# Performance work log

Hardware: AMD Instinct MI355X
Metric: run time of the kernel (lower is better)

The kernel has to match this reference:

```python
import jax, jax.numpy as jnp
import numpy as np
import math

EPS = 1e-08
KERNEL = 3
PAD = KERNEL // 2


def setup_inputs() -> dict:
    key = jax.random.key(0)
    k1, k2, k3, k4 = jax.random.split(key, 4)
    B, C_in, C_out, H, W, S = 8, 512, 512, 64, 64, 512
    x = jax.random.normal(k1, (B, C_in, H, W), dtype=jnp.float32)
    style = jax.random.normal(k2, (B, S), dtype=jnp.float32)
    # modulation Linear: kaiming_normal fan_in linear => std = 1/sqrt(S); bias filled with 1
    w_mod = jax.random.normal(k3, (C_in, S), dtype=jnp.float32) / math.sqrt(S)
    b_mod = jnp.ones((C_in,), dtype=jnp.float32)
    # conv weight: randn / sqrt(in * k^2)
    weight = jax.random.normal(k4, (1, C_out, C_in, KERNEL, KERNEL), dtype=jnp.float32) / math.sqrt(C_in * KERNEL * KERNEL)
    return {"x": x, "style": style, "w_mod": w_mod, "b_mod": b_mod, "weight": weight}


def _modconv(x, style, w_mod, b_mod, weight):
    # style modulation: (B, S) @ (S, C_in) + bias -> (B, 1, C_in, 1, 1)
    s = style @ w_mod.T + b_mod
    w = weight * s[:, None, :, None, None]            # (B, C_out, C_in, k, k)
    # demodulate: rsqrt of sum of squares over (in, kh, kw)
    demod = jax.lax.rsqrt(jnp.sum(w * w, axis=(2, 3, 4)) + EPS)  # (B, C_out)
    w = w * demod[:, :, None, None, None]

    # groups=B conv == per-sample conv; vmap over batch
    def conv1(xb, wb):
        # xb: (C_in, H, W), wb: (C_out, C_in, k, k)
        return jax.lax.conv_general_dilated(
            xb[None], wb, window_strides=(1, 1),
            padding=[(PAD, PAD), (PAD, PAD)],
            dimension_numbers=("NCHW", "OIHW", "NCHW"))[0]

    return jax.vmap(conv1)(x, w)  # (B, C_out, H, W)


def reference(x, style, w_mod, b_mod, weight):
    return _modconv(x, style, w_mod, b_mod, weight)
```

## Files before the change

### kernel.cpp

```cpp
#include <hip/hip_runtime.h>
#include <hip/hip_bf16.h>

#define BATCH 8
#define CIN   512
#define COUT  512
#define HH    64
#define WW    64
#define SS    512
#define HP    66
#define WP    66
#define NPIX  (HH*WW)

typedef __bf16 bfrag  __attribute__((ext_vector_type(8)));
typedef float  f32x4  __attribute__((ext_vector_type(4)));
typedef unsigned short u16x8 __attribute__((ext_vector_type(8)));

__device__ __forceinline__ void async_copy16(const __hip_bfloat16* g, __hip_bfloat16* l) {
    __builtin_amdgcn_global_load_lds(
        (const __attribute__((address_space(1))) void*)g,
        (__attribute__((address_space(3))) void*)l,
        16, 0, 0);
}

__device__ __forceinline__ bool is_f32(const void* b_mod) {
    return ((const unsigned int*)b_mod)[0] == 0x3F800000u;
}

__global__ void k_prep(const void* __restrict__ style,
                       const void* __restrict__ w_mod,
                       const void* __restrict__ b_mod,
                       const void* __restrict__ weight,
                       float* __restrict__ s_out,
                       float* __restrict__ wsq,
                       __hip_bfloat16* __restrict__ Wt) {
    const bool f32 = is_f32(b_mod);
    if (blockIdx.x < 1024) {
        int tid = blockIdx.x * 256 + threadIdx.x;
        float sq = 0.f;
        if (f32) {
            const float* w = (const float*)weight + (size_t)tid * 9;
#pragma unroll
            for (int k = 0; k < 9; ++k) {
                float v = w[k];
                sq += v * v;
                Wt[k * (COUT * CIN) + tid] = __float2bfloat16(v);
            }
        } else {
            const __hip_bfloat16* w = (const __hip_bfloat16*)weight + (size_t)tid * 9;
#pragma unroll
            for (int k = 0; k < 9; ++k) {
                float v = __bfloat162float(w[k]);
                sq += v * v;
                Wt[k * (COUT * CIN) + tid] = w[k];
            }
        }
        wsq[tid] = sq;
    } else {
        int gw   = (blockIdx.x - 1024) * 4 + (threadIdx.x >> 6);
        int lane = threadIdx.x & 63;
        int b = gw >> 9, i = gw & 511;
        int base = lane * 8;
        float acc = 0.f;
        if (f32) {
            const float* st = (const float*)style + b * SS + base;
            const float* wm = (const float*)w_mod + i * SS + base;
#pragma unroll
            for (int j = 0; j < 8; ++j) acc += st[j] * wm[j];
        } else {
            const __hip_bfloat16* st = (const __hip_bfloat16*)style + b * SS + base;
            const __hip_bfloat16* wm = (const __hip_bfloat16*)w_mod + i * SS + base;
#pragma unroll
            for (int j = 0; j < 8; ++j)
                acc += __bfloat162float(st[j]) * __bfloat162float(wm[j]);
        }
#pragma unroll
        for (int off = 32; off; off >>= 1) acc += __shfl_down(acc, off);
        if (lane == 0) {
            float bias = f32 ? ((const float*)b_mod)[i]
                             : __bfloat162float(((const __hip_bfloat16*)b_mod)[i]);
            s_out[gw] = acc + bias;
        }
    }
}

__global__ void k_mid(const void* __restrict__ xv,
                      const float* __restrict__ s_buf,
                      const float* __restrict__ wsq,
                      const void* __restrict__ b_mod,
                      float* __restrict__ demod,
                      int b0, int nx, int do_demod,
                      __hip_bfloat16* __restrict__ xpad) {
    if ((int)blockIdx.x >= nx) {
        if (!do_demod) return;
        int gw   = ((int)blockIdx.x - nx) * 4 + (threadIdx.x >> 6);
        int lane = threadIdx.x & 63;
        int b = gw >> 9, o = gw & 511;
        int base = lane * 8;
        const float* sp = s_buf + b * CIN + base;
        const float* wp = wsq + o * CIN + base;
        float acc = 0.f;
#pragma unroll
        for (int j = 0; j < 8; ++j) {
            float sv = sp[j];
            acc += sv * sv * wp[j];
        }
#pragma unroll
        for (int off = 32; off; off >>= 1) acc += __shfl_down(acc, off);
        if (lane == 0) demod[gw] = rsqrtf(acc + 1e-8f);
        return;
    }
    const bool f32 = is_f32(b_mod);
    int ic = blockIdx.x & 15;
    int h  = (blockIdx.x >> 4) & 63;
    int bl = blockIdx.x >> 10;
    int b  = b0 + bl;
    int t  = threadIdx.x;
    int g  = t & 3;
    int w  = t >> 2;
    int ch0 = ic * 32 + g * 8;

    float sv[8];
#pragma unroll
    for (int j = 0; j < 8; ++j) sv[j] = s_buf[b * CIN + ch0 + j];

    u16x8 outv;
#pragma unroll
    for (int j = 0; j < 8; ++j) {
        size_t src = (size_t)(b * CIN + ch0 + j) * NPIX + h * WW + w;
        float xval = f32 ? ((const float*)xv)[src]
                         : __bfloat162float(((const __hip_bfloat16*)xv)[src]);
        __hip_bfloat16 bv = __float2bfloat16(xval * sv[j]);
        outv[j] = *(unsigned short*)&bv;
    }
    size_t rowb = (size_t)(bl * HP + h + 1) * WP;
    *(u16x8*)(xpad + (rowb + (w + 1)) * CIN + ch0) = outv;

    u16x8 z = {};
    if (w == 0)  *(u16x8*)(xpad + (rowb + 0)  * CIN + ch0) = z;
    if (w == 63) *(u16x8*)(xpad + (rowb + 65) * CIN + ch0) = z;
    if (h == 0) {
        size_t r0 = (size_t)(bl * HP + 0) * WP;
        *(u16x8*)(xpad + (r0 + (w + 1)) * CIN + ch0) = z;
        if (w == 0)  *(u16x8*)(xpad + (r0 + 0)  * CIN + ch0) = z;
        if (w == 63) *(u16x8*)(xpad + (r0 + 65) * CIN + ch0) = z;
    }
    if (h == 63) {
        size_t r65 = (size_t)(bl * HP + 65) * WP;
        *(u16x8*)(xpad + (r65 + (w + 1)) * CIN + ch0) = z;
        if (w == 0)  *(u16x8*)(xpad + (r65 + 0)  * CIN + ch0) = z;
        if (w == 63) *(u16x8*)(xpad + (r65 + 65) * CIN + ch0) = z;
    }
}

__global__ __launch_bounds__(256, 2)
void k_conv(const __hip_bfloat16* __restrict__ Wt,
            const __hip_bfloat16* __restrict__ xpad,
            const float* __restrict__ demod,
            const void* __restrict__ b_mod, int b0,
            void* __restrict__ outv) {
    __shared__ __hip_bfloat16 sA[2][3][128 * 32];
    __shared__ __hip_bfloat16 sB[2][6144];

    const int tid  = threadIdx.x;
    const int wid  = tid >> 6;
    const int lane = tid & 63;
    const int p_tile = blockIdx.x;
    const int o_tile = blockIdx.y;
    const int bl     = blockIdx.z;
    const int b      = b0 + bl;

    const int o_base = o_tile * 128;
    const int h0     = p_tile * 2;
    const int p_base = p_tile * 128;

    const int sw = ((lane & 3) ^ ((lane >> 3) & 3)) * 8;

    const int arow0 = wid * 32 + (lane >> 2);
    const int arow1 = arow0 + 16;
    const int aoff0 = wid * 1024 + lane * 8;
    const int aoff1 = aoff0 + 512;
    const int asrc0 = (o_base + arow0) * CIN + sw;
    const int asrc1 = (o_base + arow1) * CIN + sw;

    int bdst[3], bsrc[3];
#pragma unroll
    for (int jj = 0; jj < 3; ++jj) {
        int j   = wid * 3 + jj;
        int pix = j * 16 + (lane >> 2);
        int pm  = pix < 131 ? pix : 131;
        int r   = (pm >= 66) ? 1 : 0;
        int c   = pm - (r ? 66 : 0);
        bdst[jj] = j * 512 + lane * 8;
        bsrc[jj] = ((bl * HP + h0 + r) * WP + c) * CIN + sw;
    }

    const int quad   = lane >> 4;
    const int l15    = lane & 15;
    const int wave_m = (wid >> 1) * 64;
    const int wave_n = (wid & 1) * 64;
    int afrag[4];
#pragma unroll
    for (int mt = 0; mt < 4; ++mt) {
        int row = wave_m + mt * 16 + l15;
        afrag[mt] = row * 32 + ((quad ^ ((l15 >> 1) & 3)) * 8);
    }
    int bfroff[4][3];
#pragma unroll
    for (int nt = 0; nt < 4; ++nt) {
        int n   = wave_n + nt * 16 + l15;
        int pr0 = (n >> 6) * 66 + (n & 63);
#pragma unroll
        for (int kw = 0; kw < 3; ++kw) {
            int pr = pr0 + kw;
            bfroff[nt][kw] = pr * 32 + ((quad ^ ((pr >> 1) & 3)) * 8);
        }
    }

    f32x4 acc[4][4];
#pragma unroll
    for (int mt = 0; mt < 4; ++mt)
#pragma unroll
        for (int nt = 0; nt < 4; ++nt)
            acc[mt][nt] = (f32x4)0.f;

    auto stage = [&](int buf, int it) {
        const int kh = it >> 4;
        const int i0 = (it & 15) << 5;
        const __hip_bfloat16* Wkh = Wt + kh * 3 * (COUT * CIN) + i0;
        const __hip_bfloat16* xr  = xpad + kh * (WP * CIN) + i0;
#pragma unroll
        for (int kw = 0; kw < 3; ++kw) {
            const __hip_bfloat16* Ap = Wkh + kw * (COUT * CIN);
            async_copy16(Ap + asrc0, &sA[buf][kw][aoff0]);
            async_copy16(Ap + asrc1, &sA[buf][kw][aoff1]);
        }
#pragma unroll
        for (int jj = 0; jj < 3; ++jj)
            async_copy16(xr + bsrc[jj], &sB[buf][bdst[jj]]);
    };

    auto compute = [&](int buf) {
        __builtin_amdgcn_s_setprio(1);
#pragma unroll
        for (int kw = 0; kw < 3; ++kw) {
            bfrag a[4], bb[4];
#pragma unroll
            for (int mt = 0; mt < 4; ++mt)
                a[mt] = *(const bfrag*)(&sA[buf][kw][afrag[mt]]);
#pragma unroll
            for (int nt = 0; nt < 4; ++nt)
                bb[nt] = *(const bfrag*)(&sB[buf][bfroff[nt][kw]]);
#pragma unroll
            for (int mt = 0; mt < 4; ++mt)
#pragma unroll
                for (int nt = 0; nt < 4; ++nt)
                    acc[mt][nt] = __builtin_amdgcn_mfma_f32_16x16x32_bf16(
                        a[mt], bb[nt], acc[mt][nt], 0, 0, 0);
        }
        __builtin_amdgcn_s_setprio(0);
    };

    stage(0, 0);
#pragma unroll 2
    for (int it = 0; it < 47; ++it) {
        stage((it + 1) & 1, it + 1);
        asm volatile("s_waitcnt vmcnt(9)" ::: "memory");
        __builtin_amdgcn_s_barrier();
        asm volatile("" ::: "memory");
        compute(it & 1);
        asm volatile("" ::: "memory");
        __builtin_amdgcn_s_barrier();
    }
    asm volatile("s_waitcnt vmcnt(0)" ::: "memory");
    __builtin_amdgcn_s_barrier();
    asm volatile("" ::: "memory");
    compute(1);

    const bool f32 = is_f32(b_mod);
#pragma unroll
    for (int mt = 0; mt < 4; ++mt) {
        const int o0r = o_base + wave_m + mt * 16 + quad * 4;
        float dm[4];
#pragma unroll
        for (int r = 0; r < 4; ++r) dm[r] = demod[b * COUT + o0r + r];
#pragma unroll
        for (int nt = 0; nt < 4; ++nt) {
            const int p = p_base + wave_n + nt * 16 + l15;
#pragma unroll
            for (int r = 0; r < 4; ++r) {
                float val = acc[mt][nt][r] * dm[r];
                size_t idx = (size_t)(b * COUT + o0r + r) * NPIX + p;
                if (f32) ((float*)outv)[idx] = val;
                else     ((__hip_bfloat16*)outv)[idx] = __float2bfloat16(val);
            }
        }
    }
}

extern "C" void kernel_launch(void* const* d_in, const int* in_sizes, int n_in,
                              void* d_out, int out_size, void* d_ws, size_t ws_size,
                              hipStream_t stream) {
    const void* x      = d_in[0];
    const void* style  = d_in[1];
    const void* w_mod  = d_in[2];
    const void* b_mod  = d_in[3];
    const void* weight = d_in[4];

    char* ws = (char*)d_ws;
    float*          s_buf = (float*)(ws + 4096);
    float*          demod = (float*)(ws + 20480);
    float*          wsq   = (float*)(ws + 36864);
    __hip_bfloat16* Wt    = (__hip_bfloat16*)(ws + 1085440);
    __hip_bfloat16* xpad  = (__hip_bfloat16*)(ws + 5804032);

    const size_t need_full = 5804032 + (size_t)BATCH * HP * WP * CIN * 2;
    const int group = (ws_size >= need_full) ? 8 : 4;

    k_prep<<<2048, 256, 0, stream>>>(style, w_mod, b_mod, weight, s_buf, wsq, Wt);

    for (int b0 = 0; b0 < BATCH; b0 += group) {
        const int nx = 1024 * group;
        const int do_demod = (b0 == 0) ? 1 : 0;
        const int nd = do_demod ? 1024 : 0;
        k_mid<<<nx + nd, 256, 0, stream>>>(x, s_buf, wsq, b_mod, demod,
                                           b0, nx, do_demod, xpad);
        k_conv<<<dim3(32, 4, group), 256, 0, stream>>>(Wt, xpad, demod, b_mod, b0, d_out);
    }
}
```

Baseline: 269.0 us.

## Load conv weight fragments directly from global memory and remap blocks per XCD

Drops the LDS staging of the modulated-weight (A) operand. Each wave now reads its A fragments straight from global memory into registers at the start of each compute step, and only the input (B) tile is still staged asynchronously through LDS. This shrinks LDS use, so the launch bound is raised to three blocks per CU. The 3D grid is also flattened into a 1D grid with an XCD-aware mapping, so that blocks sharing an output-channel tile land on the same XCD for L2 reuse. In exchange, the global A loads have no prefetch, so their latency may be exposed right before the MFMAs, and waves sharing rows issue duplicate loads.

After: 436.1 us. +62.1%, slower.

```diff
diff --git a/kernel.cpp b/kernel.cpp
--- a/kernel.cpp
+++ b/kernel.cpp
@@ -152,21 +152,24 @@
     }
 }
 
-__global__ __launch_bounds__(256, 2)
+__global__ __launch_bounds__(256, 3)
 void k_conv(const __hip_bfloat16* __restrict__ Wt,
             const __hip_bfloat16* __restrict__ xpad,
             const float* __restrict__ demod,
             const void* __restrict__ b_mod, int b0,
             void* __restrict__ outv) {
-    __shared__ __hip_bfloat16 sA[2][3][128 * 32];
     __shared__ __hip_bfloat16 sB[2][6144];
 
     const int tid  = threadIdx.x;
     const int wid  = tid >> 6;
     const int lane = tid & 63;
-    const int p_tile = blockIdx.x;
-    const int o_tile = blockIdx.y;
-    const int bl     = blockIdx.z;
+
+    const int id     = blockIdx.x;
+    const int xcd    = id & 7;
+    const int g      = id >> 3;
+    const int o_tile = xcd >> 1;
+    const int p_tile = (xcd & 1) * 16 + (g & 15);
+    const int bl     = g >> 4;
     const int b      = b0 + bl;
 
     const int o_base = o_tile * 128;
@@ -174,13 +177,6 @@
     const int p_base = p_tile * 128;
 
     const int sw = ((lane & 3) ^ ((lane >> 3) & 3)) * 8;
-
-    const int arow0 = wid * 32 + (lane >> 2);
-    const int arow1 = arow0 + 16;
-    const int aoff0 = wid * 1024 + lane * 8;
-    const int aoff1 = aoff0 + 512;
-    const int asrc0 = (o_base + arow0) * CIN + sw;
-    const int asrc1 = (o_base + arow1) * CIN + sw;
 
     int bdst[3], bsrc[3];
 #pragma unroll
@@ -198,12 +194,9 @@
     const int l15    = lane & 15;
     const int wave_m = (wid >> 1) * 64;
     const int wave_n = (wid & 1) * 64;
-    int afrag[4];
-#pragma unroll
-    for (int mt = 0; mt < 4; ++mt) {
-        int row = wave_m + mt * 16 + l15;
-        afrag[mt] = row * 32 + ((quad ^ ((l15 >> 1) & 3)) * 8);
-    }
+
+    const __hip_bfloat16* Arow = Wt + (size_t)(o_base + wave_m + l15) * CIN + quad * 8;
+
     int bfroff[4][3];
 #pragma unroll
     for (int nt = 0; nt < 4; ++nt) {
@@ -223,30 +216,29 @@
         for (int nt = 0; nt < 4; ++nt)
             acc[mt][nt] = (f32x4)0.f;
 
-    auto stage = [&](int buf, int it) {
+    auto stageB = [&](int buf, int it) {
         const int kh = it >> 4;
         const int i0 = (it & 15) << 5;
-        const __hip_bfloat16* Wkh = Wt + kh * 3 * (COUT * CIN) + i0;
-        const __hip_bfloat16* xr  = xpad + kh * (WP * CIN) + i0;
-#pragma unroll
-        for (int kw = 0; kw < 3; ++kw) {
-            const __hip_bfloat16* Ap = Wkh + kw * (COUT * CIN);
-            async_copy16(Ap + asrc0, &sA[buf][kw][aoff0]);
-            async_copy16(Ap + asrc1, &sA[buf][kw][aoff1]);
-        }
+        const __hip_bfloat16* xr = xpad + kh * (WP * CIN) + i0;
 #pragma unroll
         for (int jj = 0; jj < 3; ++jj)
             async_copy16(xr + bsrc[jj], &sB[buf][bdst[jj]]);
     };
 
-    auto compute = [&](int buf) {
+    auto compute = [&](int buf, int it) {
+        const int kh = it >> 4;
+        const int i0 = (it & 15) << 5;
+        const __hip_bfloat16* Ap = Arow + kh * 3 * (COUT * CIN) + i0;
+        bfrag a[3][4];
+#pragma unroll
+        for (int kw = 0; kw < 3; ++kw)
+#pragma unroll
+            for (int mt = 0; mt < 4; ++mt)
+                a[kw][mt] = *(const bfrag*)(Ap + kw * (COUT * CIN) + mt * 16 * CIN);
         __builtin_amdgcn_s_setprio(1);
 #pragma unroll
         for (int kw = 0; kw < 3; ++kw) {
-            bfrag a[4], bb[4];
-#pragma unroll
-            for (int mt = 0; mt < 4; ++mt)
-                a[mt] = *(const bfrag*)(&sA[buf][kw][afrag[mt]]);
+            bfrag bb[4];
 #pragma unroll
             for (int nt = 0; nt < 4; ++nt)
                 bb[nt] = *(const bfrag*)(&sB[buf][bfroff[nt][kw]]);
@@ -255,26 +247,26 @@
 #pragma unroll
                 for (int nt = 0; nt < 4; ++nt)
                     acc[mt][nt] = __builtin_amdgcn_mfma_f32_16x16x32_bf16(
-                        a[mt], bb[nt], acc[mt][nt], 0, 0, 0);
+                        a[kw][mt], bb[nt], acc[mt][nt], 0, 0, 0);
         }
         __builtin_amdgcn_s_setprio(0);
     };
 
-    stage(0, 0);
+    stageB(0, 0);
 #pragma unroll 2
     for (int it = 0; it < 47; ++it) {
-        stage((it + 1) & 1, it + 1);
-        asm volatile("s_waitcnt vmcnt(9)" ::: "memory");
+        stageB((it + 1) & 1, it + 1);
+        asm volatile("s_waitcnt vmcnt(3)" ::: "memory");
         __builtin_amdgcn_s_barrier();
         asm volatile("" ::: "memory");
-        compute(it & 1);
+        compute(it & 1, it);
         asm volatile("" ::: "memory");
         __builtin_amdgcn_s_barrier();
     }
     asm volatile("s_waitcnt vmcnt(0)" ::: "memory");
     __builtin_amdgcn_s_barrier();
     asm volatile("" ::: "memory");
-    compute(1);
+    compute(1, 47);
 
     const bool f32 = is_f32(b_mod);
 #pragma unroll
@@ -324,6 +316,6 @@
         const int nd = do_demod ? 1024 : 0;
         k_mid<<<nx + nd, 256, 0, stream>>>(x, s_buf, wsq, b_mod, demod,
                                            b0, nx, do_demod, xpad);
-        k_conv<<<dim3(32, 4, group), 256, 0, stream>>>(Wt, xpad, demod, b_mod, b0, d_out);
-    }
-}
+        k_conv<<<dim3(128 * group), 256, 0, stream>>>(Wt, xpad, demod, b_mod, b0, d_out);
+    }
+}
```
